# Kernel tuning notes

Hardware: AMD Instinct MI355X
Metric: run time of the kernel (lower is better)

## Reference

```python
import jax, jax.numpy as jnp
import numpy as np
import math

# module hyperparameters (init_kwargs)
C_H = 128
K = 8
INP_SIZE = 256
S_MIN = 1.0
S_MAX_OOD = 30.0
SIGMA = 0.8
BQ = 131072


def setup_inputs() -> dict:
    key = jax.random.key(0)
    k1, k2, k3 = jax.random.split(key, 3)
    h = jax.random.normal(k1, (BQ, C_H, K), dtype=jnp.float32)
    cell = jax.random.uniform(k2, (BQ, 2), dtype=jnp.float32)
    # kaiming_uniform with a=sqrt(5) on a [3, C_h] weight -> bound = 1/sqrt(C_h)
    bound = 1.0 / math.sqrt(C_H)
    to_rgb_weight = jax.random.uniform(k3, (K, 3, C_H), dtype=jnp.float32,
                                       minval=-bound, maxval=bound)
    to_rgb_bias = jnp.zeros((K, 3), dtype=jnp.float32)
    return {"h": h, "cell": cell, "to_rgb_weight": to_rgb_weight,
            "to_rgb_bias": to_rgb_bias}


def reference(h, cell, to_rgb_weight, to_rgb_bias):
    # tau: [BQ]
    cell_geomean = jnp.maximum(jnp.sqrt(cell[:, 0] * cell[:, 1]), 1e-10)
    log_s = math.log(2.0 / INP_SIZE) - jnp.log(cell_geomean)
    tau = (K - 1) * (log_s - math.log(S_MIN)) / (math.log(S_MAX_OOD) - math.log(S_MIN))
    tau = jnp.clip(tau, 0.0, K - 1)

    # alpha: [BQ, K] Gaussian softmax over scales
    k_idx = jnp.arange(K, dtype=jnp.float32)[None, :]            # [1, K]
    logits = -(k_idx - tau[:, None]) ** 2 / (2.0 * SIGMA ** 2)   # [BQ, K]
    alpha = jax.nn.softmax(logits, axis=1)

    # per-k projection C_h -> 3: h is [BQ, C_h, K]
    rgb_k = jnp.einsum('bck,koc->bko', h, to_rgb_weight) + to_rgb_bias[None]  # [BQ, K, 3]
    y_eq = jnp.sum(alpha[:, :, None] * rgb_k, axis=1)            # [BQ, 3]
    return y_eq
```

## Files before the change

kernel.cpp:

```cpp
#include <hip/hip_runtime.h>
#include <math.h>


#define C_H   128
#define KSC   8

constexpr int NBLOCKS  = 2048;
constexpr int NTHREADS = 256;
constexpr int NWAVES   = NBLOCKS * NTHREADS / 64;

__global__ __launch_bounds__(NTHREADS)
void gsr_kernel(const float* __restrict__ h,
                const float* __restrict__ cell,
                const float* __restrict__ w,
                const float* __restrict__ bias,
                float* __restrict__ out,
                int bq)
{
    const int lane   = threadIdx.x & 63;
    const int waveId = blockIdx.x * (NTHREADS / 64) + (threadIdx.x >> 6);

    const int kbase = (lane & 1) * 4;
    const int chalf = lane >> 1;
    float wreg[16][3];
    #pragma unroll
    for (int i = 0; i < 4; ++i) {
        #pragma unroll
        for (int e = 0; e < 4; ++e) {
            const int k = kbase + e;
            const int c = i * 32 + chalf;
            #pragma unroll
            for (int o = 0; o < 3; ++o)
                wreg[i*4+e][o] = w[k * (3*C_H) + o * C_H + c];
        }
    }
    float breg[4][3];
    #pragma unroll
    for (int e = 0; e < 4; ++e)
        #pragma unroll
        for (int o = 0; o < 3; ++o)
            breg[e][o] = (lane < 2) ? bias[(kbase + e) * 3 + o] : 0.0f;

    const float inv_two_sigma_sq = 0.78125f;
    const float log_2_over_inp   = -4.8520302639196171f;
    const float seven_over_log30 = 2.0580814087539097f;

    for (int b = waveId; b < bq; b += NWAVES) {
        const float c0 = cell[2*b + 0];
        const float c1 = cell[2*b + 1];
        const float geo = fmaxf(sqrtf(c0 * c1), 1e-10f);
        const float log_s = log_2_over_inp - __logf(geo);
        float tau = seven_over_log30 * log_s;
        tau = fminf(fmaxf(tau, 0.0f), 7.0f);

        float ek[8], s = 0.0f;
        #pragma unroll
        for (int k = 0; k < 8; ++k) {
            const float d = (float)k - tau;
            ek[k] = __expf(-d * d * inv_two_sigma_sq);
            s += ek[k];
        }
        const float inv = 1.0f / s;
        float al[4];
        #pragma unroll
        for (int e = 0; e < 4; ++e)
            al[e] = ((lane & 1) ? ek[4 + e] : ek[e]) * inv;

        const float4* hp = (const float4*)(h + (size_t)b * (C_H * KSC));
        float4 hv[4];
        #pragma unroll
        for (int i = 0; i < 4; ++i)
            hv[i] = hp[i * 64 + lane];

        float acc[3];
        #pragma unroll
        for (int o = 0; o < 3; ++o) {
            acc[o] = al[0] * breg[0][o];
            #pragma unroll
            for (int e = 1; e < 4; ++e)
                acc[o] = fmaf(al[e], breg[e][o], acc[o]);
        }
        #pragma unroll
        for (int i = 0; i < 4; ++i) {
            const float he[4] = {hv[i].x, hv[i].y, hv[i].z, hv[i].w};
            #pragma unroll
            for (int e = 0; e < 4; ++e) {
                const float ha = he[e] * al[e];
                #pragma unroll
                for (int o = 0; o < 3; ++o)
                    acc[o] = fmaf(ha, wreg[i*4+e][o], acc[o]);
            }
        }

        #pragma unroll
        for (int off = 32; off > 0; off >>= 1) {
            acc[0] += __shfl_xor(acc[0], off, 64);
            acc[1] += __shfl_xor(acc[1], off, 64);
            acc[2] += __shfl_xor(acc[2], off, 64);
        }

        if (lane == 0) {
            out[(size_t)b * 3 + 0] = acc[0];
            out[(size_t)b * 3 + 1] = acc[1];
            out[(size_t)b * 3 + 2] = acc[2];
        }
    }
}

extern "C" void kernel_launch(void* const* d_in, const int* in_sizes, int n_in,
                              void* d_out, int out_size, void* d_ws, size_t ws_size,
                              hipStream_t stream) {
    const float* h    = (const float*)d_in[0];
    const float* cell = (const float*)d_in[1];
    const float* w    = (const float*)d_in[2];
    const float* bias = (const float*)d_in[3];
    float* out = (float*)d_out;
    const int bq = in_sizes[0] / (C_H * KSC);

    gsr_kernel<<<NBLOCKS, NTHREADS, 0, stream>>>(h, cell, w, bias, out, bq);
}
```

Before: 690.2 us.

## Map one thread per query with LDS-staged weights and register double-buffering

Replaces the one-wavefront-per-query grid-stride scheme with one thread per query. The projection weights are staged in shared memory, and each thread streams its own 4 KB slice of h in 128-byte chunks with software prefetch into registers. This removes the cross-lane shuffle reduction and the per-query softmax work that every lane repeated. In exchange, h loads become strided across lanes by 4 KB, so memory coalescing is lost, and the large per-thread register footprint limits occupancy.

```diff
diff --git a/kernel.cpp b/kernel.cpp
--- a/kernel.cpp
+++ b/kernel.cpp
@@ -4,12 +4,9 @@
 
 #define C_H   128
 #define KSC   8
+#define QBLK  256
 
-constexpr int NBLOCKS  = 2048;
-constexpr int NTHREADS = 256;
-constexpr int NWAVES   = NBLOCKS * NTHREADS / 64;
-
-__global__ __launch_bounds__(NTHREADS)
+__global__ __launch_bounds__(QBLK)
 void gsr_kernel(const float* __restrict__ h,
                 const float* __restrict__ cell,
                 const float* __restrict__ w,
@@ -17,94 +14,91 @@
                 float* __restrict__ out,
                 int bq)
 {
-    const int lane   = threadIdx.x & 63;
-    const int waveId = blockIdx.x * (NTHREADS / 64) + (threadIdx.x >> 6);
+    __shared__ float W2[256 * 12];
+    __shared__ float B2[24];
 
-    const int kbase = (lane & 1) * 4;
-    const int chalf = lane >> 1;
-    float wreg[16][3];
-    #pragma unroll
-    for (int i = 0; i < 4; ++i) {
+    const int t = threadIdx.x;
+
+    {
+        const int i  = t;
+        const int kh = i & 1;
+        const int c  = i >> 1;
         #pragma unroll
-        for (int e = 0; e < 4; ++e) {
-            const int k = kbase + e;
-            const int c = i * 32 + chalf;
+        for (int e = 0; e < 4; ++e)
             #pragma unroll
             for (int o = 0; o < 3; ++o)
-                wreg[i*4+e][o] = w[k * (3*C_H) + o * C_H + c];
-        }
+                W2[i * 12 + e * 3 + o] = w[(kh * 4 + e) * (3 * C_H) + o * C_H + c];
+        if (t < 24) B2[t] = bias[t];
     }
-    float breg[4][3];
-    #pragma unroll
-    for (int e = 0; e < 4; ++e)
-        #pragma unroll
-        for (int o = 0; o < 3; ++o)
-            breg[e][o] = (lane < 2) ? bias[(kbase + e) * 3 + o] : 0.0f;
+    __syncthreads();
+
+    const int b = blockIdx.x * QBLK + t;
+    if (b >= bq) return;
 
     const float inv_two_sigma_sq = 0.78125f;
     const float log_2_over_inp   = -4.8520302639196171f;
     const float seven_over_log30 = 2.0580814087539097f;
 
-    for (int b = waveId; b < bq; b += NWAVES) {
-        const float c0 = cell[2*b + 0];
-        const float c1 = cell[2*b + 1];
-        const float geo = fmaxf(sqrtf(c0 * c1), 1e-10f);
-        const float log_s = log_2_over_inp - __logf(geo);
-        float tau = seven_over_log30 * log_s;
-        tau = fminf(fmaxf(tau, 0.0f), 7.0f);
+    const float2 cg = ((const float2*)cell)[b];
+    const float geo = fmaxf(sqrtf(cg.x * cg.y), 1e-10f);
+    const float log_s = log_2_over_inp - __logf(geo);
+    float tau = seven_over_log30 * log_s;
+    tau = fminf(fmaxf(tau, 0.0f), 7.0f);
 
-        float ek[8], s = 0.0f;
+    float al[8], s = 0.0f;
+    #pragma unroll
+    for (int k = 0; k < 8; ++k) {
+        const float d = (float)k - tau;
+        al[k] = __expf(-d * d * inv_two_sigma_sq);
+        s += al[k];
+    }
+    const float inv = 1.0f / s;
+    #pragma unroll
+    for (int k = 0; k < 8; ++k) al[k] *= inv;
+
+    float acc[3];
+    #pragma unroll
+    for (int o = 0; o < 3; ++o) {
+        float a0 = 0.0f;
         #pragma unroll
-        for (int k = 0; k < 8; ++k) {
-            const float d = (float)k - tau;
-            ek[k] = __expf(-d * d * inv_two_sigma_sq);
-            s += ek[k];
+        for (int k = 0; k < 8; ++k)
+            a0 = fmaf(al[k], B2[k * 3 + o], a0);
+        acc[o] = a0;
+    }
+
+    const float4* hp = (const float4*)(h + (size_t)b * (C_H * KSC));
+    float4 cur[8], nxt[8];
+    #pragma unroll
+    for (int u = 0; u < 8; ++u) cur[u] = hp[u];
+
+    for (int ch = 0; ch < 32; ++ch) {
+        if (ch < 31) {
+            #pragma unroll
+            for (int u = 0; u < 8; ++u) nxt[u] = hp[(ch + 1) * 8 + u];
         }
-        const float inv = 1.0f / s;
-        float al[4];
+        const int ibase = ch * 8;
         #pragma unroll
-        for (int e = 0; e < 4; ++e)
-            al[e] = ((lane & 1) ? ek[4 + e] : ek[e]) * inv;
-
-        const float4* hp = (const float4*)(h + (size_t)b * (C_H * KSC));
-        float4 hv[4];
-        #pragma unroll
-        for (int i = 0; i < 4; ++i)
-            hv[i] = hp[i * 64 + lane];
-
-        float acc[3];
-        #pragma unroll
-        for (int o = 0; o < 3; ++o) {
-            acc[o] = al[0] * breg[0][o];
-            #pragma unroll
-            for (int e = 1; e < 4; ++e)
-                acc[o] = fmaf(al[e], breg[e][o], acc[o]);
-        }
-        #pragma unroll
-        for (int i = 0; i < 4; ++i) {
-            const float he[4] = {hv[i].x, hv[i].y, hv[i].z, hv[i].w};
+        for (int u = 0; u < 8; ++u) {
+            const int kh = u & 1;
+            const float* wrow = &W2[(ibase + u) * 12];
+            const float he[4] = {cur[u].x, cur[u].y, cur[u].z, cur[u].w};
             #pragma unroll
             for (int e = 0; e < 4; ++e) {
-                const float ha = he[e] * al[e];
+                const float ha = he[e] * al[kh * 4 + e];
                 #pragma unroll
                 for (int o = 0; o < 3; ++o)
-                    acc[o] = fmaf(ha, wreg[i*4+e][o], acc[o]);
+                    acc[o] = fmaf(ha, wrow[e * 3 + o], acc[o]);
             }
         }
-
-        #pragma unroll
-        for (int off = 32; off > 0; off >>= 1) {
-            acc[0] += __shfl_xor(acc[0], off, 64);
-            acc[1] += __shfl_xor(acc[1], off, 64);
-            acc[2] += __shfl_xor(acc[2], off, 64);
-        }
-
-        if (lane == 0) {
-            out[(size_t)b * 3 + 0] = acc[0];
-            out[(size_t)b * 3 + 1] = acc[1];
-            out[(size_t)b * 3 + 2] = acc[2];
+        if (ch < 31) {
+            #pragma unroll
+            for (int u = 0; u < 8; ++u) cur[u] = nxt[u];
         }
     }
+
+    out[(size_t)b * 3 + 0] = acc[0];
+    out[(size_t)b * 3 + 1] = acc[1];
+    out[(size_t)b * 3 + 2] = acc[2];
 }
 
 extern "C" void kernel_launch(void* const* d_in, const int* in_sizes, int n_in,
@@ -117,5 +111,6 @@
     float* out = (float*)d_out;
     const int bq = in_sizes[0] / (C_H * KSC);
 
-    gsr_kernel<<<NBLOCKS, NTHREADS, 0, stream>>>(h, cell, w, bias, out, bq);
+    const int nblocks = (bq + QBLK - 1) / QBLK;
+    gsr_kernel<<<nblocks, QBLK, 0, stream>>>(h, cell, w, bias, out, bq);
 }
```

Result: slower. 721.9 us (+4.6%).
